# Kernel tuning notes

Measured on AMD Instinct MI355X. Metric: run time of the kernel, lower is better.

## Reference

```python
import jax, jax.numpy as jnp
import numpy as np

D_MODEL = 96
D_EXP = 192      # d_expand == d_inner (ssm_ratio=ssm_rank_ratio=2)
D_STATE = 16
DT_RANK = 6      # ceil(96/16)
DC_IN = 4        # dc_inner
DC_STATE = 16
DTC_RANK = 6
B, H, W = 2, 48, 48


def _ln_channel(x, w, b):
    # WithBias LayerNorm over channel dim (torch code reshapes b c h w -> b (hw) c)
    mu = x.mean(axis=1, keepdims=True)
    var = ((x - mu) ** 2).mean(axis=1, keepdims=True)
    return (x - mu) / jnp.sqrt(var + 1e-5) * w[None, :, None, None] + b[None, :, None, None]


def _selective_scan(u, delta, A, Bs, Cs, D, delta_bias):
    # u, delta: (b,k,d,l); A: (k,d,n); Bs,Cs: (b,k,n,l); D, delta_bias: (k,d)
    delta = jax.nn.softplus(delta + delta_bias[None, :, :, None])
    dA = jnp.exp(jnp.einsum('bkdl,kdn->bkldn', delta, A))          # decay per step
    dBu = jnp.einsum('bkdl,bkdl,bknl->bkldn', delta, u, Bs)        # input injection

    def combine(c1, c2):
        a1, b1 = c1
        a2, b2 = c2
        return a1 * a2, a2 * b1 + b2

    _, hs = jax.lax.associative_scan(combine, (dA, dBu), axis=2)   # parallel linear recurrence over l
    return jnp.einsum('bkldn,bknl->bkdl', hs, Cs) + D[None, :, :, None] * u


def _spatial_core(x, x_proj_w, dt_w, dt_b, A_logs, Ds, onw, onb):
    b, d, h, w = x.shape
    l = h * w
    # cross_scan_2d: row-major, col-major, and their flips -> (b,4,d,l)
    xs = jnp.stack([x.reshape(b, d, l), jnp.swapaxes(x, 2, 3).reshape(b, d, l)], 1)
    xs = jnp.concatenate([xs, jnp.flip(xs, -1)], 1)
    x_dbl = jnp.einsum('bkdl,kcd->bkcl', xs, x_proj_w)
    dts, Bs, Cs = jnp.split(x_dbl, [DT_RANK, DT_RANK + D_STATE], axis=2)
    dts = jnp.einsum('bkrl,kdr->bkdl', dts, dt_w)
    A = -jnp.exp(A_logs).reshape(4, d, D_STATE)
    out_y = _selective_scan(xs, dts, A, Bs, Cs, Ds.reshape(4, d), dt_b)  # (b,4,d,l)
    inv = jnp.flip(out_y[:, 2:4], -1)
    wh = jnp.swapaxes(out_y[:, 1].reshape(b, d, w, h), 2, 3).reshape(b, d, l)
    invwh = jnp.swapaxes(inv[:, 1].reshape(b, d, w, h), 2, 3).reshape(b, d, l)
    y = (out_y[:, 0] + inv[:, 0] + wh + invwh).reshape(b, d, h, w)
    return _ln_channel(y, onw, onb)


def _channel_core(y, cin_w, cin_b, cout_w, cout_b, xc_proj_w, dtc_w, dtc_b, Ac_logs, Dsc, cnw, cnb):
    b, d = y.shape[0], y.shape[1]
    xc = y.mean(axis=(2, 3))                                              # adaptive avg pool -> (b,d)
    xc = xc[:, None, :] * cin_w.reshape(1, DC_IN, 1) + cin_b.reshape(1, DC_IN, 1)  # 1x1 conv_cin -> (b,4,d)
    xsc = jnp.stack([xc, jnp.flip(xc, -1)], 1)                            # (b,2,dc,L=d)
    xc_dbl = jnp.einsum('bkdl,kcd->bkcl', xsc, xc_proj_w)
    dtsc, Bc, Cc = jnp.split(xc_dbl, [DTC_RANK, DTC_RANK + DC_STATE], axis=2)
    dtsc = jnp.einsum('bkrl,kdr->bkdl', dtsc, dtc_w)
    Ac = -jnp.exp(Ac_logs).reshape(2, DC_IN, DC_STATE)
    outc = _selective_scan(xsc, dtsc, Ac, Bc, Cc, Dsc.reshape(2, DC_IN), dtc_b)  # (b,2,dc,d)
    yc = outc[:, 0] + jnp.flip(outc[:, 1], -1)                            # merge fwd/bwd channel scans
    yc = jnp.einsum('bdl,d->bl', yc, cout_w.reshape(DC_IN)) + cout_b.reshape(())  # 1x1 conv_cout
    return _ln_channel(yc.reshape(b, d, 1, 1), cnw, cnb)


def _conv1x1(x, w, b):
    return jnp.einsum('bchw,oc->bohw', x, w.reshape(w.shape[0], w.shape[1])) + b[None, :, None, None]


def _forward(x, in_w, in_b, dw_w, dw_b, x_proj_w, dt_w, dt_b, A_logs, Ds, out_norm_w, out_norm_b,
             cin_w, cin_b, cout_w, cout_b, xc_proj_w, dtc_w, dtc_b, Ac_logs, Dsc, cn_w, cn_b,
             out_w, out_b):
    xz = _conv1x1(x, in_w, in_b)                      # (b, 2*d_expand, h, w)
    x1, z = xz[:, :D_EXP], xz[:, D_EXP:]
    z = jax.nn.silu(z)
    x1 = jax.lax.conv_general_dilated(x1, dw_w, (1, 1), 'SAME',
                                      dimension_numbers=('NCHW', 'OIHW', 'NCHW'),
                                      feature_group_count=D_EXP) + dw_b[None, :, None, None]
    x1 = jax.nn.silu(x1)
    y = _spatial_core(x1, x_proj_w, dt_w, dt_b, A_logs, Ds, out_norm_w, out_norm_b)
    c = _channel_core(y, cin_w, cin_b, cout_w, cout_b, xc_proj_w, dtc_w, dtc_b, Ac_logs, Dsc, cn_w, cn_b)
    y = y * c * z                                     # channel modulation + gating
    return _conv1x1(y, out_w, out_b)


def setup_inputs():
    key = jax.random.key(0)
    ks = jax.random.split(key, 24)
    s = 0.02

    def rn(k, shape, scale=s):
        return jax.random.normal(k, shape, jnp.float32) * scale

    A_logs = jnp.log(jnp.tile(jnp.arange(1, D_STATE + 1, dtype=jnp.float32)[None, :], (4 * D_EXP, 1)))
    return dict(
        x=jax.random.normal(ks[0], (B, D_MODEL, H, W), jnp.float32),
        in_w=rn(ks[1], (2 * D_EXP, D_MODEL, 1, 1)),
        in_b=rn(ks[2], (2 * D_EXP,)),
        dw_w=rn(ks[3], (D_EXP, 1, 3, 3)),
        dw_b=rn(ks[4], (D_EXP,)),
        x_proj_w=rn(ks[5], (4, DT_RANK + 2 * D_STATE, D_EXP)),
        dt_w=rn(ks[6], (4, D_EXP, DT_RANK), 0.1),
        dt_b=rn(ks[7], (4, D_EXP), 0.5) - 4.0,
        A_logs=A_logs,
        Ds=jnp.ones((4 * D_EXP,), jnp.float32),
        out_norm_w=jnp.ones((D_EXP,), jnp.float32),
        out_norm_b=jnp.zeros((D_EXP,), jnp.float32),
        cin_w=rn(ks[8], (DC_IN, 1, 1, 1), 0.5),
        cin_b=rn(ks[9], (DC_IN,), 0.1),
        cout_w=rn(ks[10], (1, DC_IN, 1, 1), 0.5),
        cout_b=rn(ks[11], (1,), 0.1),
        xc_proj_w=rn(ks[12], (2, DTC_RANK + 2 * DC_STATE, DC_IN), 0.2),
        dtc_w=rn(ks[13], (2, DC_IN, DTC_RANK), 0.2),
        dtc_b=rn(ks[14], (2, DC_IN), 0.5),
        Ac_logs=rn(ks[15], (2 * DC_IN, DC_STATE), 1.0),
        Dsc=jnp.ones((2 * DC_IN,), jnp.float32),
        cn_w=jnp.ones((D_EXP,), jnp.float32),
        cn_b=jnp.zeros((D_EXP,), jnp.float32),
        out_w=rn(ks[16], (D_MODEL, D_EXP, 1, 1)),
        out_b=rn(ks[17], (D_MODEL,)),
    )


def reference(x, in_w, in_b, dw_w, dw_b, x_proj_w, dt_w, dt_b, A_logs, Ds, out_norm_w, out_norm_b,
              cin_w, cin_b, cout_w, cout_b, xc_proj_w, dtc_w, dtc_b, Ac_logs, Dsc, cn_w, cn_b,
              out_w, out_b):
    return _forward(x, in_w, in_b, dw_w, dw_b, x_proj_w, dt_w, dt_b, A_logs, Ds, out_norm_w, out_norm_b,
                    cin_w, cin_b, cout_w, cout_b, xc_proj_w, dtc_w, dtc_b, Ac_logs, Dsc, cn_w, cn_b,
                    out_w, out_b)
```

## Files before the change

### kernel.cpp

```cpp
#include <hip/hip_runtime.h>
#include <math.h>

#define DM 96
#define DE 192
#define LL 2304
#define NS 16
#define RK 6
#define NC 38
#define CH4 64
#define CL4 36

__device__ __forceinline__ float silu_f(float x){ return x / (1.f + __expf(-x)); }
__device__ __forceinline__ float softplus_f(float x){
  return (x > 20.f) ? x : __logf(1.f + __expf(x));
}

__device__ __forceinline__ int dir_map(int k, int l){
    switch(k){
      case 0: return l;
      case 1: return (l % 48) * 48 + l / 48;
      case 2: return 2303 - l;
      default: { int lr = 2303 - l; return (lr % 48) * 48 + lr / 48; }
    }
}

__global__ __launch_bounds__(384) void k1_conv_in(const float* __restrict__ x,
    const float* __restrict__ in_w, const float* __restrict__ in_b,
    float* __restrict__ x1raw, float* __restrict__ z){
  __shared__ float xv[DM*16];
  int tile = blockIdx.x;
  int b = tile / 144;
  int pos0 = (tile % 144) * 16;
  int tid = threadIdx.x;
  {
    int c = tid >> 2, p4 = tid & 3;
    float4 v = *(const float4*)(x + (b*DM + c)*LL + pos0 + p4*4);
    *(float4*)&xv[c*16 + p4*4] = v;
  }
  __syncthreads();
  float acc[16];
  #pragma unroll
  for (int p=0;p<16;p++) acc[p] = in_b[tid];
  const float4* wv4 = (const float4*)(in_w + tid*DM);
  #pragma unroll 4
  for (int c4=0;c4<24;c4++){
    float4 wv = wv4[c4];
    #pragma unroll
    for (int cc=0;cc<4;cc++){
      float w = (cc==0)?wv.x:((cc==1)?wv.y:((cc==2)?wv.z:wv.w));
      const float* xr = &xv[(c4*4+cc)*16];
      #pragma unroll
      for (int p4=0;p4<4;p4++){
        float4 xq = *(const float4*)&xr[p4*4];
        acc[p4*4+0] = fmaf(w, xq.x, acc[p4*4+0]);
        acc[p4*4+1] = fmaf(w, xq.y, acc[p4*4+1]);
        acc[p4*4+2] = fmaf(w, xq.z, acc[p4*4+2]);
        acc[p4*4+3] = fmaf(w, xq.w, acc[p4*4+3]);
      }
    }
  }
  if (tid < DE){
    float* dst = x1raw + (b*DE + tid)*LL + pos0;
    #pragma unroll
    for (int p4=0;p4<4;p4++)
      *(float4*)(dst + p4*4) = make_float4(acc[p4*4+0],acc[p4*4+1],acc[p4*4+2],acc[p4*4+3]);
  } else {
    int zc = tid - DE;
    float* dst = z + (b*DE + zc)*LL + pos0;
    #pragma unroll
    for (int p4=0;p4<4;p4++)
      *(float4*)(dst + p4*4) = make_float4(silu_f(acc[p4*4+0]),silu_f(acc[p4*4+1]),
                                           silu_f(acc[p4*4+2]),silu_f(acc[p4*4+3]));
  }
}

__global__ __launch_bounds__(256) void k2_dwconv(const float* __restrict__ x1raw,
    const float* __restrict__ dw_w, const float* __restrict__ dw_b,
    float* __restrict__ xconv, float* __restrict__ xconvT){
  __shared__ float lin[50][52];
  __shared__ float lout[48][50];
  int bd = blockIdx.x;
  int d = bd % DE;
  int tid = threadIdx.x;
  for (int i = tid; i < 50*52; i += 256) ((float*)lin)[i] = 0.f;
  __syncthreads();
  const float* src = x1raw + bd*LL;
  for (int i = tid; i < 576; i += 256){
    int r = i/12, c4 = (i%12)*4;
    float4 v = *(const float4*)(src + r*48 + c4);
    lin[r+1][c4+1] = v.x; lin[r+1][c4+2] = v.y; lin[r+1][c4+3] = v.z; lin[r+1][c4+4] = v.w;
  }
  float w00=dw_w[d*9+0], w01=dw_w[d*9+1], w02=dw_w[d*9+2];
  float w10=dw_w[d*9+3], w11=dw_w[d*9+4], w12=dw_w[d*9+5];
  float w20=dw_w[d*9+6], w21=dw_w[d*9+7], w22=dw_w[d*9+8];
  float bias = dw_b[d];
  __syncthreads();
  float* dst = xconv + bd*LL;
  for (int i = tid; i < 576; i += 256){
    int h = i/12, w4 = (i%12)*4;
    float o[4];
    #pragma unroll
    for (int j=0;j<4;j++){
      int w = w4 + j;
      float acc = bias;
      acc = fmaf(w00, lin[h  ][w], fmaf(w01, lin[h  ][w+1], fmaf(w02, lin[h  ][w+2], acc)));
      acc = fmaf(w10, lin[h+1][w], fmaf(w11, lin[h+1][w+1], fmaf(w12, lin[h+1][w+2], acc)));
      acc = fmaf(w20, lin[h+2][w], fmaf(w21, lin[h+2][w+1], fmaf(w22, lin[h+2][w+2], acc)));
      float v = silu_f(acc);
      o[j] = v;
      lout[h][w] = v;
    }
    *(float4*)(dst + h*48 + w4) = make_float4(o[0],o[1],o[2],o[3]);
  }
  __syncthreads();
  float* dstT = xconvT + bd*LL;
  for (int i = tid; i < 576; i += 256){
    int tw = i/12, th4 = (i%12)*4;
    float4 v = make_float4(lout[th4][tw], lout[th4+1][tw], lout[th4+2][tw], lout[th4+3][tw]);
    *(float4*)(dstT + tw*48 + th4) = v;
  }
}

__global__ __launch_bounds__(256) void k3_proj(const float* __restrict__ xconv,
    const float* __restrict__ xconvT,
    const float* __restrict__ x_proj_w, const float* __restrict__ dt_w,
    const float* __restrict__ dt_b, float* __restrict__ delta,
    float* __restrict__ B2, float* __restrict__ C2){
  __shared__ float smem[38*256];
  __shared__ float red[38*64];
  int bk = blockIdx.x / 36;
  int tile = blockIdx.x % 36;
  int b = bk >> 2, k = bk & 3;
  int tid = threadIdx.x;
  int lsub = tid & 63, dgrp = tid >> 6;
  int l = tile*64 + lsub;
  const float* wsrc = x_proj_w + k*NC*DE;
  for (int idx = tid; idx < NC*DE; idx += 256){
    int c = idx / DE, d = idx % DE;
    smem[d*40 + c] = wsrc[idx];
  }
  if (tid < DE){ smem[tid*40 + 38] = 0.f; smem[tid*40 + 39] = 0.f; }
  __syncthreads();
  float acc[40];
  #pragma unroll
  for (int c=0;c<40;c++) acc[c]=0.f;
  const float* uptr;
  {
    const float* basep = (k & 1) ? (xconvT + b*DE*LL) : (xconv + b*DE*LL);
    uptr = basep + ((k >= 2) ? (2303 - l) : l);
  }
  for (int dd=0; dd<48; dd++){
    int d = dgrp*48 + dd;
    float u = uptr[d*LL];
    const float4* wrow = (const float4*)&smem[d*40];
    #pragma unroll
    for (int j=0;j<10;j++){
      float4 wv = wrow[j];
      acc[j*4+0] = fmaf(u, wv.x, acc[j*4+0]);
      acc[j*4+1] = fmaf(u, wv.y, acc[j*4+1]);
      acc[j*4+2] = fmaf(u, wv.z, acc[j*4+2]);
      acc[j*4+3] = fmaf(u, wv.w, acc[j*4+3]);
    }
  }
  __syncthreads();
  #pragma unroll
  for (int c=0;c<38;c++) smem[c*256 + dgrp*64 + lsub] = acc[c];
  __syncthreads();
  for (int idx = tid; idx < 38*64; idx += 256){
    int c = idx >> 6, l2 = idx & 63;
    red[c*64 + l2] = smem[c*256 + l2] + smem[c*256 + 64 + l2]
                   + smem[c*256 + 128 + l2] + smem[c*256 + 192 + l2];
  }
  __syncthreads();
  {
    int l2 = tid >> 2, ng = tid & 3;
    int lg = tile*64 + l2;
    int so = (lg % 36)*64 + (lg / 36);
    float4 bv, cv;
    bv.x = red[(RK + ng*4 + 0)*64 + l2];
    bv.y = red[(RK + ng*4 + 1)*64 + l2];
    bv.z = red[(RK + ng*4 + 2)*64 + l2];
    bv.w = red[(RK + ng*4 + 3)*64 + l2];
    cv.x = red[(RK + NS + ng*4 + 0)*64 + l2];
    cv.y = red[(RK + NS + ng*4 + 1)*64 + l2];
    cv.z = red[(RK + NS + ng*4 + 2)*64 + l2];
    cv.w = red[(RK + NS + ng*4 + 3)*64 + l2];
    *(float4*)(B2 + bk*36864 + so*16 + ng*4) = bv;
    *(float4*)(C2 + bk*36864 + so*16 + ng*4) = cv;
  }
  float r0 = red[0*64 + lsub], r1 = red[1*64 + lsub], r2 = red[2*64 + lsub];
  float r3 = red[3*64 + lsub], r4 = red[4*64 + lsub], r5 = red[5*64 + lsub];
  const float* dwb = dt_w + k*DE*RK;
  const float* dbb = dt_b + k*DE;
  for (int dd=0; dd<48; dd++){
    int d = dgrp*48 + dd;
    const float* wr = dwb + d*RK;
    float t = dbb[d];
    t = fmaf(r0, wr[0], t); t = fmaf(r1, wr[1], t); t = fmaf(r2, wr[2], t);
    t = fmaf(r3, wr[3], t); t = fmaf(r4, wr[4], t); t = fmaf(r5, wr[5], t);
    delta[(bk*DE + d)*LL + l] = softplus_f(t);
  }
}

__global__ __launch_bounds__(256) void k4_scan(const float* __restrict__ xconv,
    const float* __restrict__ xconvT,
    const float* __restrict__ delta, const float* __restrict__ B2,
    const float* __restrict__ C2, const float* __restrict__ A_logs,
    const float* __restrict__ Ds, float* __restrict__ out_y){
  __shared__ float smem[3*LL];
  float* us  = smem;
  float* ds  = smem + LL;
  float* sPf = smem + 2*LL;
  float* sSf = smem + 2*LL + 1024;
  float* oyf = smem + 2*LL;
  int gid = blockIdx.x;
  int b = gid / (4*DE);
  int kd = gid % (4*DE);
  int k = kd / DE;
  int d = kd % DE;
  int bk = b*4 + k;
  int tid = threadIdx.x;
  int c = tid >> 2, q = tid & 3;
  const float LOG2E = 1.44269504f;
  float4 al = *(const float4*)&A_logs[(k*DE + d)*NS + q*4];
  float A2[4];
  A2[0] = -__expf(al.x)*LOG2E; A2[1] = -__expf(al.y)*LOG2E;
  A2[2] = -__expf(al.z)*LOG2E; A2[3] = -__expf(al.w)*LOG2E;
  float Dv = Ds[k*DE + d];
  {
    const float4* ub4 = (const float4*)(((k & 1) ? xconvT : xconv) + (b*DE + d)*LL);
    const float4* db4 = (const float4*)(delta + (bk*DE + d)*LL);
    float4* us4 = (float4*)us;
    float4* ds4 = (float4*)ds;
    for (int j = tid; j < LL/4; j += 256){ us4[j] = ub4[j]; ds4[j] = db4[j]; }
  }
  const float* bbase = B2 + bk*36864 + q*4;
  const float* cbase = C2 + bk*36864 + q*4;
  bool rev = (k >= 2);
  int l0 = c*CL4;
  __syncthreads();
  float sumdl = 0.f, S[4] = {0.f,0.f,0.f,0.f};
  #pragma unroll 4
  for (int i=0;i<CL4;i++){
    int l = l0 + i;
    float dl = ds[l];
    float u  = us[rev ? (2303 - l) : l];
    float du = dl*u;
    sumdl += dl;
    float4 Bv = *(const float4*)(bbase + (i*64 + c)*16);
    float dA0 = exp2f(dl*A2[0]); S[0] = fmaf(S[0], dA0, du*Bv.x);
    float dA1 = exp2f(dl*A2[1]); S[1] = fmaf(S[1], dA1, du*Bv.y);
    float dA2 = exp2f(dl*A2[2]); S[2] = fmaf(S[2], dA2, du*Bv.z);
    float dA3 = exp2f(dl*A2[3]); S[3] = fmaf(S[3], dA3, du*Bv.w);
  }
  *(float4*)&sPf[c*NS + q*4] = make_float4(exp2f(A2[0]*sumdl), exp2f(A2[1]*sumdl),
                                           exp2f(A2[2]*sumdl), exp2f(A2[3]*sumdl));
  *(float4*)&sSf[c*NS + q*4] = make_float4(S[0],S[1],S[2],S[3]);
  __syncthreads();
  if (tid < NS){
    float hacc = 0.f;
    #pragma unroll 4
    for (int cc=0; cc<CH4; cc++){
      hacc = fmaf(hacc, sPf[cc*NS + tid], sSf[cc*NS + tid]);
      sSf[cc*NS + tid] = hacc;
    }
  }
  __syncthreads();
  float h[4];
  if (c == 0){ h[0]=h[1]=h[2]=h[3]=0.f; }
  else { float4 hi = *(const float4*)&sSf[(c-1)*NS + q*4]; h[0]=hi.x; h[1]=hi.y; h[2]=hi.z; h[3]=hi.w; }
  __syncthreads();
  #pragma unroll 2
  for (int i=0;i<CL4;i++){
    int l = l0 + i;
    float dl = ds[l];
    float u  = us[rev ? (2303 - l) : l];
    float du = dl*u;
    float4 Bv = *(const float4*)(bbase + (i*64 + c)*16);
    float4 Cv = *(const float4*)(cbase + (i*64 + c)*16);
    float dA0 = exp2f(dl*A2[0]); h[0] = fmaf(h[0], dA0, du*Bv.x);
    float dA1 = exp2f(dl*A2[1]); h[1] = fmaf(h[1], dA1, du*Bv.y);
    float dA2 = exp2f(dl*A2[2]); h[2] = fmaf(h[2], dA2, du*Bv.z);
    float dA3 = exp2f(dl*A2[3]); h[3] = fmaf(h[3], dA3, du*Bv.w);
    float py = h[0]*Cv.x + h[1]*Cv.y + h[2]*Cv.z + h[3]*Cv.w;
    py += __shfl_xor(py, 1);
    py += __shfl_xor(py, 2);
    if (q == 0){
      oyf[dir_map(k, l)] = fmaf(Dv, u, py);
    }
  }
  __syncthreads();
  {
    float4* o4 = (float4*)(out_y + (bk*DE + d)*LL);
    const float4* s4 = (const float4*)oyf;
    for (int i = tid; i < LL/4; i += 256) o4[i] = s4[i];
  }
}

__global__ __launch_bounds__(256) void k5_combine(const float* __restrict__ out_y,
    float* __restrict__ ycomb, float* __restrict__ mu_g, float* __restrict__ rs_g,
    float* __restrict__ partial){
  __shared__ float vals[DE][17];
  __shared__ float s_[16][16], s2_[16][16];
  __shared__ float mu_[16], rs_[16];
  int bT = blockIdx.x;
  int b = bT / 144;
  int pos0 = (bT % 144) * 16;
  int tid = threadIdx.x;
  int p = tid & 15, g = tid >> 4;
  const float* base = out_y + b*4*DE*LL;
  float s = 0.f, s2 = 0.f;
  #pragma unroll
  for (int j=0;j<12;j++){
    int d = g*12 + j;
    int idx = d*LL + pos0 + p;
    float v = base[idx] + base[DE*LL + idx] + base[2*DE*LL + idx] + base[3*DE*LL + idx];
    vals[d][p] = v;
    s += v; s2 += v*v;
  }
  s_[g][p] = s; s2_[g][p] = s2;
  __syncthreads();
  if (tid < 16){
    float ss = 0.f, ss2 = 0.f;
    #pragma unroll
    for (int gg=0; gg<16; gg++){ ss += s_[gg][tid]; ss2 += s2_[gg][tid]; }
    float mu = ss / DE;
    float var = ss2 / DE - mu*mu;
    mu_[tid] = mu; rs_[tid] = rsqrtf(var + 1e-5f);
    mu_g[b*LL + pos0 + tid] = mu;
    rs_g[b*LL + pos0 + tid] = rs_[tid];
  }
  __syncthreads();
  #pragma unroll
  for (int j=0;j<12;j++){
    int d = g*12 + j;
    ycomb[(b*DE + d)*LL + pos0 + p] = vals[d][p];
  }
  __syncthreads();
  if (tid < DE){
    float ps = 0.f;
    #pragma unroll
    for (int pp=0;pp<16;pp++) ps += (vals[tid][pp] - mu_[pp]) * rs_[pp];
    partial[bT*DE + tid] = ps;
  }
}

__global__ __launch_bounds__(512) void k6b_channel(const float* __restrict__ partial,
    const float* __restrict__ onw, const float* __restrict__ onb,
    const float* __restrict__ cin_w, const float* __restrict__ cin_b,
    const float* __restrict__ cout_w, const float* __restrict__ cout_b,
    const float* __restrict__ xc_proj_w, const float* __restrict__ dtc_w,
    const float* __restrict__ dtc_b, const float* __restrict__ Ac_logs,
    const float* __restrict__ Dsc, const float* __restrict__ cn_w,
    const float* __restrict__ cn_b, float* __restrict__ cvec){
  __shared__ float xcs[DE];
  __shared__ float tmp[384];
  __shared__ float sP[128][4], sS[128][4];
  __shared__ float outc[2][4][DE];
  __shared__ float ycs[DE];
  __shared__ float muS, rsS;
  int b = blockIdx.x;
  int tid = threadIdx.x;
  if (tid < 384){
    int d = tid % DE, half = tid / DE;
    const float* pp = partial + (b*144 + half*72)*DE + d;
    float sacc = 0.f;
    #pragma unroll 8
    for (int t=0;t<72;t++) sacc += pp[t*DE];
    tmp[tid] = sacc;
  }
  __syncthreads();
  if (tid < DE) xcs[tid] = fmaf(onw[tid], (tmp[tid] + tmp[tid + DE]) * (1.f/LL), onb[tid]);
  __syncthreads();
  int chain = tid >> 2, ch = tid & 3;
  int k = chain >> 6, dc = (chain >> 4) & 3, n = chain & 15;
  const float LOG2E = 1.44269504f;
  float EW0=0,EW1=0,EW2=0,EW3=0;
  #pragma unroll
  for (int r=0;r<RK;r++){
    float dw = dtc_w[(k*4+dc)*RK + r];
    EW0 = fmaf(dw, xc_proj_w[(k*NC + r)*4 + 0], EW0);
    EW1 = fmaf(dw, xc_proj_w[(k*NC + r)*4 + 1], EW1);
    EW2 = fmaf(dw, xc_proj_w[(k*NC + r)*4 + 2], EW2);
    EW3 = fmaf(dw, xc_proj_w[(k*NC + r)*4 + 3], EW3);
  }
  float Bw0 = xc_proj_w[(k*NC + RK + n)*4 + 0];
  float Bw1 = xc_proj_w[(k*NC + RK + n)*4 + 1];
  float Bw2 = xc_proj_w[(k*NC + RK + n)*4 + 2];
  float Bw3 = xc_proj_w[(k*NC + RK + n)*4 + 3];
  float Cw0 = xc_proj_w[(k*NC + RK + NS + n)*4 + 0];
  float Cw1 = xc_proj_w[(k*NC + RK + NS + n)*4 + 1];
  float Cw2 = xc_proj_w[(k*NC + RK + NS + n)*4 + 2];
  float Cw3 = xc_proj_w[(k*NC + RK + NS + n)*4 + 3];
  float A2 = -__expf(Ac_logs[(k*4+dc)*NS + n]) * LOG2E;
  float Dv = Dsc[k*4+dc];
  float dtb = dtc_b[k*4+dc];
  float ciw0=cin_w[0], ciw1=cin_w[1], ciw2=cin_w[2], ciw3=cin_w[3];
  float cib0=cin_b[0], cib1=cin_b[1], cib2=cin_b[2], cib3=cin_b[3];
  int l0 = ch*48;
  float P = 1.f, S = 0.f;
  for (int i=0;i<48;i++){
    int lc = l0 + i;
    int lp = k ? (191 - lc) : lc;
    float xv = xcs[lp];
    float xs0 = fmaf(xv, ciw0, cib0);
    float xs1 = fmaf(xv, ciw1, cib1);
    float xs2 = fmaf(xv, ciw2, cib2);
    float xs3 = fmaf(xv, ciw3, cib3);
    float dt = dtb + xs0*EW0 + xs1*EW1 + xs2*EW2 + xs3*EW3;
    float dl = softplus_f(dt);
    float Bv = xs0*Bw0 + xs1*Bw1 + xs2*Bw2 + xs3*Bw3;
    float u = (dc==0)?xs0:((dc==1)?xs1:((dc==2)?xs2:xs3));
    float dA = exp2f(dl * A2);
    S = fmaf(S, dA, dl*u*Bv);
    P *= dA;
  }
  sP[chain][ch] = P; sS[chain][ch] = S;
  __syncthreads();
  if (tid < 128){
    float hacc = 0.f;
    #pragma unroll
    for (int cc=0; cc<4; cc++){
      hacc = fmaf(hacc, sP[tid][cc], sS[tid][cc]);
      sS[tid][cc] = hacc;
    }
  }
  __syncthreads();
  float h = (ch == 0) ? 0.f : sS[chain][ch-1];
  for (int i=0;i<48;i++){
    int lc = l0 + i;
    int lp = k ? (191 - lc) : lc;
    float xv = xcs[lp];
    float xs0 = fmaf(xv, ciw0, cib0);
    float xs1 = fmaf(xv, ciw1, cib1);
    float xs2 = fmaf(xv, ciw2, cib2);
    float xs3 = fmaf(xv, ciw3, cib3);
    float dt = dtb + xs0*EW0 + xs1*EW1 + xs2*EW2 + xs3*EW3;
    float dl = softplus_f(dt);
    float Bv = xs0*Bw0 + xs1*Bw1 + xs2*Bw2 + xs3*Bw3;
    float Cv = xs0*Cw0 + xs1*Cw1 + xs2*Cw2 + xs3*Cw3;
    float u = (dc==0)?xs0:((dc==1)?xs1:((dc==2)?xs2:xs3));
    float dA = exp2f(dl * A2);
    h = fmaf(h, dA, dl*u*Bv);
    float py = h * Cv;
    py += __shfl_xor(py, 4);
    py += __shfl_xor(py, 8);
    py += __shfl_xor(py, 16);
    py += __shfl_xor(py, 32);
    if (n == 0) outc[k][dc][lc] = fmaf(Dv, u, py);
  }
  __syncthreads();
  float co0=cout_w[0], co1=cout_w[1], co2=cout_w[2], co3=cout_w[3], cob=cout_b[0];
  for (int i = tid; i < DE; i += 512){
    float yv = cob
      + co0*(outc[0][0][i] + outc[1][0][191-i])
      + co1*(outc[0][1][i] + outc[1][1][191-i])
      + co2*(outc[0][2][i] + outc[1][2][191-i])
      + co3*(outc[0][3][i] + outc[1][3][191-i]);
    ycs[i] = yv;
  }
  __syncthreads();
  if (tid < 64){
    float s = 0.f, s2 = 0.f;
    #pragma unroll
    for (int j=0;j<3;j++){
      float v = ycs[tid + j*64];
      s += v; s2 += v*v;
    }
    for (int off=32; off>0; off>>=1){ s += __shfl_down(s, off); s2 += __shfl_down(s2, off); }
    if (tid == 0){
      float mu = s / DE;
      float var = s2 / DE - mu*mu;
      muS = mu; rsS = rsqrtf(var + 1e-5f);
    }
  }
  __syncthreads();
  float mu = muS, rs = rsS;
  for (int i = tid; i < DE; i += 512){
    cvec[b*DE + i] = (ycs[i] - mu) * rs * cn_w[i] + cn_b[i];
  }
}

__global__ __launch_bounds__(256) void k7_out(const float* __restrict__ ycomb,
    const float* __restrict__ mu_g, const float* __restrict__ rs_g,
    const float* __restrict__ onw, const float* __restrict__ onb,
    const float* __restrict__ cvec, const float* __restrict__ z,
    const float* __restrict__ out_w, const float* __restrict__ out_b,
    float* __restrict__ outp){
  __shared__ float t[DE*16];
  int tile = blockIdx.x;
  int b = tile / 144;
  int pos0 = (tile % 144) * 16;
  int tid = threadIdx.x;
  for (int i = tid; i < DE*4; i += 256){
    int c = i >> 2, p4 = (i & 3)*4;
    int gi = (b*DE + c)*LL + pos0 + p4;
    float4 yv = *(const float4*)(ycomb + gi);
    float4 zv = *(const float4*)(z + gi);
    float4 m4 = *(const float4*)(mu_g + b*LL + pos0 + p4);
    float4 r4 = *(const float4*)(rs_g + b*LL + pos0 + p4);
    float w = onw[c], bb = onb[c];
    float cv = cvec[b*DE + c];
    float t0 = fmaf((yv.x - m4.x)*r4.x, w, bb) * cv * zv.x;
    float t1 = fmaf((yv.y - m4.y)*r4.y, w, bb) * cv * zv.y;
    float t2 = fmaf((yv.z - m4.z)*r4.z, w, bb) * cv * zv.z;
    float t3 = fmaf((yv.w - m4.w)*r4.w, w, bb) * cv * zv.w;
    *(float4*)&t[c*16 + p4] = make_float4(t0,t1,t2,t3);
  }
  __syncthreads();
  for (int j = tid; j < DM*16; j += 256){
    int o = j >> 4, p = j & 15;
    float acc = out_b[o];
    const float4* wr4 = (const float4*)(out_w + o*DE);
    #pragma unroll 8
    for (int c4=0;c4<48;c4++){
      float4 wv = wr4[c4];
      acc = fmaf(wv.x, t[(c4*4+0)*16+p], acc);
      acc = fmaf(wv.y, t[(c4*4+1)*16+p], acc);
      acc = fmaf(wv.z, t[(c4*4+2)*16+p], acc);
      acc = fmaf(wv.w, t[(c4*4+3)*16+p], acc);
    }
    outp[(b*DM + o)*LL + pos0 + p] = acc;
  }
}

extern "C" void kernel_launch(void* const* d_in, const int* in_sizes, int n_in,
                              void* d_out, int out_size, void* d_ws, size_t ws_size,
                              hipStream_t stream){
  const float* x        = (const float*)d_in[0];
  const float* in_w     = (const float*)d_in[1];
  const float* in_b     = (const float*)d_in[2];
  const float* dw_w     = (const float*)d_in[3];
  const float* dw_b     = (const float*)d_in[4];
  const float* x_proj_w = (const float*)d_in[5];
  const float* dt_w     = (const float*)d_in[6];
  const float* dt_b     = (const float*)d_in[7];
  const float* A_logs   = (const float*)d_in[8];
  const float* Ds       = (const float*)d_in[9];
  const float* onw      = (const float*)d_in[10];
  const float* onb      = (const float*)d_in[11];
  const float* cin_w    = (const float*)d_in[12];
  const float* cin_b    = (const float*)d_in[13];
  const float* cout_w   = (const float*)d_in[14];
  const float* cout_b   = (const float*)d_in[15];
  const float* xc_proj_w= (const float*)d_in[16];
  const float* dtc_w    = (const float*)d_in[17];
  const float* dtc_b    = (const float*)d_in[18];
  const float* Ac_logs  = (const float*)d_in[19];
  const float* Dsc      = (const float*)d_in[20];
  const float* cn_w     = (const float*)d_in[21];
  const float* cn_b     = (const float*)d_in[22];
  const float* out_w    = (const float*)d_in[23];
  const float* out_b    = (const float*)d_in[24];

  float* ws = (float*)d_ws;
  float* x1raw = ws;  ws += 2*DE*LL;
  float* zbuf  = ws;  ws += 2*DE*LL;
  float* xconv = ws;  ws += 2*DE*LL;
  float* xconvT= ws;  ws += 2*DE*LL;
  float* delta = ws;  ws += 2*4*DE*LL;
  float* B2    = ws;  ws += 2*4*LL*NS;
  float* C2    = ws;  ws += 2*4*LL*NS;
  float* outy  = ws;  ws += 2*4*DE*LL;
  float* ycomb = ws;  ws += 2*DE*LL;
  float* cvec  = ws;  ws += 2*DE;
  float* partial = ws; ws += 2*144*DE;
  float* mu_g  = ws;  ws += 2*LL;
  float* rs_g  = ws;  ws += 2*LL;

  hipLaunchKernelGGL(k1_conv_in, dim3(288), dim3(384), 0, stream, x, in_w, in_b, x1raw, zbuf);
  hipLaunchKernelGGL(k2_dwconv, dim3(384), dim3(256), 0, stream, x1raw, dw_w, dw_b, xconv, xconvT);
  hipLaunchKernelGGL(k3_proj, dim3(288), dim3(256), 0, stream, xconv, xconvT, x_proj_w, dt_w, dt_b, delta, B2, C2);
  hipLaunchKernelGGL(k4_scan, dim3(1536), dim3(256), 0, stream, xconv, xconvT, delta, B2, C2, A_logs, Ds, outy);
  hipLaunchKernelGGL(k5_combine, dim3(288), dim3(256), 0, stream, outy, ycomb, mu_g, rs_g, partial);
  hipLaunchKernelGGL(k6b_channel, dim3(2), dim3(512), 0, stream, partial, onw, onb, cin_w, cin_b, cout_w, cout_b,
                     xc_proj_w, dtc_w, dtc_b, Ac_logs, Dsc, cn_w, cn_b, cvec);
  hipLaunchKernelGGL(k7_out, dim3(288), dim3(256), 0, stream, ycomb, mu_g, rs_g, onw, onb, cvec, zbuf, out_w, out_b, (float*)d_out);
}
```

Before: 170.3 us.

## Pair forward/reverse scan directions per block and pre-sum their outputs

Each scan block now has 512 threads and handles two directions (k and k+2) that share the same input sequence. The input is loaded into shared memory once, and the two direction outputs are summed in shared memory before being written to one of two planes. The combine kernel then reads two planes instead of four and no longer writes a combined buffer; the output kernel sums the two planes itself. This cuts global memory traffic for the scan outputs and the ycomb round trip, in exchange for larger shared memory per block (5*LL floats) and bigger blocks, which may lower occupancy.

```diff
diff --git a/kernel.cpp b/kernel.cpp
--- a/kernel.cpp
+++ b/kernel.cpp
@@ -202,25 +202,30 @@
   }
 }
 
-__global__ __launch_bounds__(256) void k4_scan(const float* __restrict__ xconv,
+__global__ __launch_bounds__(512) void k4_scan(const float* __restrict__ xconv,
     const float* __restrict__ xconvT,
     const float* __restrict__ delta, const float* __restrict__ B2,
     const float* __restrict__ C2, const float* __restrict__ A_logs,
-    const float* __restrict__ Ds, float* __restrict__ out_y){
-  __shared__ float smem[3*LL];
-  float* us  = smem;
-  float* ds  = smem + LL;
-  float* sPf = smem + 2*LL;
-  float* sSf = smem + 2*LL + 1024;
-  float* oyf = smem + 2*LL;
+    const float* __restrict__ Ds, float* __restrict__ planeA,
+    float* __restrict__ planeB){
+  __shared__ float smem[5*LL];
+  float* us = smem;
+  float* X  = smem + 3*LL;
   int gid = blockIdx.x;
-  int b = gid / (4*DE);
-  int kd = gid % (4*DE);
-  int k = kd / DE;
-  int d = kd % DE;
+  int b = gid / (2*DE);
+  int rem = gid % (2*DE);
+  int pairId = rem / DE;
+  int d = rem % DE;
+  int tid = threadIdx.x;
+  int kg = tid >> 8;
+  int sub = tid & 255;
+  int c = sub >> 2, q = sub & 3;
+  int k = pairId + kg*2;
   int bk = b*4 + k;
-  int tid = threadIdx.x;
-  int c = tid >> 2, q = tid & 3;
+  float* ds  = smem + LL + kg*LL;
+  float* sPf = X + kg*2048;
+  float* sSf = X + kg*2048 + 1024;
+  float* oyf = X + kg*LL;
   const float LOG2E = 1.44269504f;
   float4 al = *(const float4*)&A_logs[(k*DE + d)*NS + q*4];
   float A2[4];
@@ -228,15 +233,16 @@
   A2[2] = -__expf(al.z)*LOG2E; A2[3] = -__expf(al.w)*LOG2E;
   float Dv = Ds[k*DE + d];
   {
-    const float4* ub4 = (const float4*)(((k & 1) ? xconvT : xconv) + (b*DE + d)*LL);
+    const float4* ub4 = (const float4*)((pairId ? xconvT : xconv) + (b*DE + d)*LL);
+    float4* us4 = (float4*)us;
+    for (int j = tid; j < LL/4; j += 512) us4[j] = ub4[j];
     const float4* db4 = (const float4*)(delta + (bk*DE + d)*LL);
-    float4* us4 = (float4*)us;
     float4* ds4 = (float4*)ds;
-    for (int j = tid; j < LL/4; j += 256){ us4[j] = ub4[j]; ds4[j] = db4[j]; }
+    for (int j = sub; j < LL/4; j += 256) ds4[j] = db4[j];
   }
   const float* bbase = B2 + bk*36864 + q*4;
   const float* cbase = C2 + bk*36864 + q*4;
-  bool rev = (k >= 2);
+  bool rev = (kg == 1);
   int l0 = c*CL4;
   __syncthreads();
   float sumdl = 0.f, S[4] = {0.f,0.f,0.f,0.f};
@@ -257,12 +263,12 @@
                                            exp2f(A2[2]*sumdl), exp2f(A2[3]*sumdl));
   *(float4*)&sSf[c*NS + q*4] = make_float4(S[0],S[1],S[2],S[3]);
   __syncthreads();
-  if (tid < NS){
+  if (sub < NS){
     float hacc = 0.f;
     #pragma unroll 4
     for (int cc=0; cc<CH4; cc++){
-      hacc = fmaf(hacc, sPf[cc*NS + tid], sSf[cc*NS + tid]);
-      sSf[cc*NS + tid] = hacc;
+      hacc = fmaf(hacc, sPf[cc*NS + sub], sSf[cc*NS + sub]);
+      sSf[cc*NS + sub] = hacc;
     }
   }
   __syncthreads();
@@ -291,14 +297,20 @@
   }
   __syncthreads();
   {
-    float4* o4 = (float4*)(out_y + (bk*DE + d)*LL);
-    const float4* s4 = (const float4*)oyf;
-    for (int i = tid; i < LL/4; i += 256) o4[i] = s4[i];
-  }
-}
-
-__global__ __launch_bounds__(256) void k5_combine(const float* __restrict__ out_y,
-    float* __restrict__ ycomb, float* __restrict__ mu_g, float* __restrict__ rs_g,
+    float* plane = (pairId ? planeB : planeA) + (b*DE + d)*LL;
+    const float4* s0 = (const float4*)(X);
+    const float4* s1 = (const float4*)(X + LL);
+    float4* o4 = (float4*)plane;
+    for (int i = tid; i < LL/4; i += 512){
+      float4 a = s0[i], e = s1[i];
+      o4[i] = make_float4(a.x+e.x, a.y+e.y, a.z+e.z, a.w+e.w);
+    }
+  }
+}
+
+__global__ __launch_bounds__(256) void k5_stats(const float* __restrict__ planeA,
+    const float* __restrict__ planeB,
+    float* __restrict__ mu_g, float* __restrict__ rs_g,
     float* __restrict__ partial){
   __shared__ float vals[DE][17];
   __shared__ float s_[16][16], s2_[16][16];
@@ -308,13 +320,12 @@
   int pos0 = (bT % 144) * 16;
   int tid = threadIdx.x;
   int p = tid & 15, g = tid >> 4;
-  const float* base = out_y + b*4*DE*LL;
   float s = 0.f, s2 = 0.f;
   #pragma unroll
   for (int j=0;j<12;j++){
     int d = g*12 + j;
-    int idx = d*LL + pos0 + p;
-    float v = base[idx] + base[DE*LL + idx] + base[2*DE*LL + idx] + base[3*DE*LL + idx];
+    int idx = (b*DE + d)*LL + pos0 + p;
+    float v = planeA[idx] + planeB[idx];
     vals[d][p] = v;
     s += v; s2 += v*v;
   }
@@ -329,12 +340,6 @@
     mu_[tid] = mu; rs_[tid] = rsqrtf(var + 1e-5f);
     mu_g[b*LL + pos0 + tid] = mu;
     rs_g[b*LL + pos0 + tid] = rs_[tid];
-  }
-  __syncthreads();
-  #pragma unroll
-  for (int j=0;j<12;j++){
-    int d = g*12 + j;
-    ycomb[(b*DE + d)*LL + pos0 + p] = vals[d][p];
   }
   __syncthreads();
   if (tid < DE){
@@ -481,7 +486,8 @@
   }
 }
 
-__global__ __launch_bounds__(256) void k7_out(const float* __restrict__ ycomb,
+__global__ __launch_bounds__(256) void k7_out(const float* __restrict__ planeA,
+    const float* __restrict__ planeB,
     const float* __restrict__ mu_g, const float* __restrict__ rs_g,
     const float* __restrict__ onw, const float* __restrict__ onb,
     const float* __restrict__ cvec, const float* __restrict__ z,
@@ -495,16 +501,17 @@
   for (int i = tid; i < DE*4; i += 256){
     int c = i >> 2, p4 = (i & 3)*4;
     int gi = (b*DE + c)*LL + pos0 + p4;
-    float4 yv = *(const float4*)(ycomb + gi);
+    float4 av = *(const float4*)(planeA + gi);
+    float4 ev = *(const float4*)(planeB + gi);
     float4 zv = *(const float4*)(z + gi);
     float4 m4 = *(const float4*)(mu_g + b*LL + pos0 + p4);
     float4 r4 = *(const float4*)(rs_g + b*LL + pos0 + p4);
     float w = onw[c], bb = onb[c];
     float cv = cvec[b*DE + c];
-    float t0 = fmaf((yv.x - m4.x)*r4.x, w, bb) * cv * zv.x;
-    float t1 = fmaf((yv.y - m4.y)*r4.y, w, bb) * cv * zv.y;
-    float t2 = fmaf((yv.z - m4.z)*r4.z, w, bb) * cv * zv.z;
-    float t3 = fmaf((yv.w - m4.w)*r4.w, w, bb) * cv * zv.w;
+    float t0 = fmaf((av.x+ev.x - m4.x)*r4.x, w, bb) * cv * zv.x;
+    float t1 = fmaf((av.y+ev.y - m4.y)*r4.y, w, bb) * cv * zv.y;
+    float t2 = fmaf((av.z+ev.z - m4.z)*r4.z, w, bb) * cv * zv.z;
+    float t3 = fmaf((av.w+ev.w - m4.w)*r4.w, w, bb) * cv * zv.w;
     *(float4*)&t[c*16 + p4] = make_float4(t0,t1,t2,t3);
   }
   __syncthreads();
@@ -561,8 +568,8 @@
   float* delta = ws;  ws += 2*4*DE*LL;
   float* B2    = ws;  ws += 2*4*LL*NS;
   float* C2    = ws;  ws += 2*4*LL*NS;
-  float* outy  = ws;  ws += 2*4*DE*LL;
-  float* ycomb = ws;  ws += 2*DE*LL;
+  float* planeA= ws;  ws += 2*DE*LL;
+  float* planeB= ws;  ws += 2*DE*LL;
   float* cvec  = ws;  ws += 2*DE;
   float* partial = ws; ws += 2*144*DE;
   float* mu_g  = ws;  ws += 2*LL;
@@ -571,9 +578,9 @@
   hipLaunchKernelGGL(k1_conv_in, dim3(288), dim3(384), 0, stream, x, in_w, in_b, x1raw, zbuf);
   hipLaunchKernelGGL(k2_dwconv, dim3(384), dim3(256), 0, stream, x1raw, dw_w, dw_b, xconv, xconvT);
   hipLaunchKernelGGL(k3_proj, dim3(288), dim3(256), 0, stream, xconv, xconvT, x_proj_w, dt_w, dt_b, delta, B2, C2);
-  hipLaunchKernelGGL(k4_scan, dim3(1536), dim3(256), 0, stream, xconv, xconvT, delta, B2, C2, A_logs, Ds, outy);
-  hipLaunchKernelGGL(k5_combine, dim3(288), dim3(256), 0, stream, outy, ycomb, mu_g, rs_g, partial);
+  hipLaunchKernelGGL(k4_scan, dim3(768), dim3(512), 0, stream, xconv, xconvT, delta, B2, C2, A_logs, Ds, planeA, planeB);
+  hipLaunchKernelGGL(k5_stats, dim3(288), dim3(256), 0, stream, planeA, planeB, mu_g, rs_g, partial);
   hipLaunchKernelGGL(k6b_channel, dim3(2), dim3(512), 0, stream, partial, onw, onb, cin_w, cin_b, cout_w, cout_b,
                      xc_proj_w, dtc_w, dtc_b, Ac_logs, Dsc, cn_w, cn_b, cvec);
-  hipLaunchKernelGGL(k7_out, dim3(288), dim3(256), 0, stream, ycomb, mu_g, rs_g, onw, onb, cvec, zbuf, out_w, out_b, (float*)d_out);
-}
+  hipLaunchKernelGGL(k7_out, dim3(288), dim3(256), 0, stream, planeA, planeB, mu_g, rs_g, onw, onb, cvec, zbuf, out_w, out_b, (float*)d_out);
+}
```

Measured after the change: 171.7 us. About the same (+0.8%).
